# Kernel optimization log

Hardware: AMD Instinct MI355X
Metric: run time of the kernel (lower is better)

## Reference

```python
import jax, jax.numpy as jnp
import numpy as np
from math import sqrt

NUM_CLASSES = 21
TOP_K = 200
CONF_THRESH = 0.01
NMS_THRESH = 0.45
VAR0, VAR1 = 0.1, 0.2
FMAPS = [19, 10, 5, 3, 2, 1]
INPUT_SIZE = 300
STEPS = [16, 32, 64, 100, 150, 300]
MIN_SIZES = [60, 105, 150, 195, 240, 285]
MAX_SIZES = [105, 150, 195, 240, 285, 330]
ASPECT_RATIOS = [[2, 3]] * 6


def _create_priorbox():
    # Faithful numpy port of create_priorbox (runs once at setup).
    mean = []
    for k, f in enumerate(FMAPS):
        f_k = INPUT_SIZE / STEPS[k]
        s_k = MIN_SIZES[k] / INPUT_SIZE
        s_kp = sqrt(s_k * (MAX_SIZES[k] / INPUT_SIZE))
        for i in range(f):
            for j in range(f):
                cx = (j + 0.5) / f_k
                cy = (i + 0.5) / f_k
                mean.append([cx, cy, s_k, s_k])
                mean.append([cx, cy, s_kp, s_kp])
                for ar in ASPECT_RATIOS[k]:
                    r = sqrt(ar)
                    mean.append([cx, cy, s_k * r, s_k / r])
                    mean.append([cx, cy, s_k / r, s_k * r])
    return np.clip(np.asarray(mean, dtype=np.float32), 0.0, 1.0)  # [3000, 4]


def setup_inputs() -> dict:
    key = jax.random.key(0)
    k1, k2 = jax.random.split(key)
    B, P, C = 8, 3000, NUM_CLASSES
    loc_data = jax.random.normal(k1, (B, P, 4), jnp.float32)
    conf_data = jax.random.uniform(k2, (B, P, C), jnp.float32)  # post-softmax-like probs
    priors = jnp.asarray(_create_priorbox())
    return {"loc_data": loc_data, "conf_data": conf_data, "priors": priors}


def _decode(loc, priors):
    # SSD box decode: center-offset form -> corner form. loc, priors: [P, 4]
    cxcy = priors[:, :2] + loc[:, :2] * VAR0 * priors[:, 2:]
    wh = priors[:, 2:] * jnp.exp(loc[:, 2:] * VAR1)
    xy1 = cxcy - 0.5 * wh
    return jnp.concatenate([xy1, xy1 + wh], axis=-1)  # [P, 4] (x1, y1, x2, y2)


def _iou_matrix(b):
    # b: [P, 4] corner-form boxes -> [P, P] pairwise IoU
    area = (b[:, 2] - b[:, 0]) * (b[:, 3] - b[:, 1])
    lt = jnp.maximum(b[:, None, :2], b[None, :, :2])
    rb = jnp.minimum(b[:, None, 2:], b[None, :, 2:])
    wh = jnp.clip(rb - lt, 0.0)
    inter = wh[..., 0] * wh[..., 1]
    union = area[:, None] + area[None, :] - inter
    return inter / jnp.maximum(union, 1e-12)


def _nms_one_class(scores, boxes):
    # scores: [P], boxes: [P, 4]. Greedy hard NMS over threshold-passing boxes,
    # kept detections (in score order) padded to TOP_K rows of [score, x1, y1, x2, y2].
    P = scores.shape[0]
    valid = scores > CONF_THRESH
    s = jnp.where(valid, scores, -jnp.inf)
    order = jnp.argsort(-s)  # descending by score; invalid sorted last
    ss = s[order]
    sb = boxes[order]
    sv = valid[order]
    iou = _iou_matrix(sb)  # [P, P]
    idx = jnp.arange(P)

    def body(i, keep):
        sup = keep[i] & (iou[i] > NMS_THRESH) & (idx > i)
        return keep & ~sup

    keep = jax.lax.stop_gradient(jax.lax.fori_loop(0, P, body, sv))
    # first TOP_K kept candidates, preserving score order
    sel = jnp.argsort(jnp.where(keep, idx, idx + P))[:TOP_K]
    ok = keep[sel]
    out_s = jnp.where(ok, ss[sel], 0.0)
    out_b = jnp.where(ok[:, None], sb[sel], 0.0)
    return jnp.concatenate([out_s[:, None], out_b], axis=-1)  # [TOP_K, 5]


def _per_image(loc, conf, priors):
    boxes = _decode(loc, priors)  # [P, 4]
    cls_scores = conf.T[1:]  # skip background class 0 -> [C-1, P]
    dets = jax.vmap(lambda s: _nms_one_class(s, boxes))(cls_scores)  # [C-1, TOP_K, 5]
    bg = jnp.zeros((1, TOP_K, 5), dets.dtype)
    return jnp.concatenate([bg, dets], axis=0)  # [C, TOP_K, 5]


def reference(loc_data, conf_data, priors):
    # lax.map over batch keeps peak memory to one image's IoU matrices.
    # NOTE: the original's final flt[(rank < top_k)].fill_(0) is a no-op in
    # PyTorch (advanced indexing returns a copy), so output is returned as-is.
    out = jax.lax.map(lambda lc: _per_image(lc[0], lc[1], priors), (loc_data, conf_data))
    return out  # [B, NUM_CLASSES, TOP_K, 5]
```

## Files before the change

### kernel.cpp

```cpp
#include <hip/hip_runtime.h>
#include <math.h>

#pragma clang fp contract(off)

#define PNUM    3000
#define NCLS    21
#define TOPK    200
#define BLOCK   1024
#define CHUNK   1024
#define NMS_T   0.45f
#define LO_BITS 0x3C23D70Bu
#define HI_BITS 0x3F800001u
#define MAXKEEP (TOPK + 64)

__device__ __constant__ unsigned LADDER[15] = {
    0x3F333333u, 0x3F266666u, 0x3F19999Au, 0x3F0CCCCDu, 0x3F000000u,
    0x3EE66666u, 0x3ECCCCCDu, 0x3EB33333u, 0x3E99999Au, 0x3E800000u,
    0x3E4CCCCDu, 0x3E19999Au, 0x3DCCCCCDu, 0x3D4CCCCDu, LO_BITS };

__device__ __forceinline__ float iou_f(float4 a, float aa, float4 b, float ab) {
    float ltx = fmaxf(a.x, b.x);
    float lty = fmaxf(a.y, b.y);
    float rbx = fminf(a.z, b.z);
    float rby = fminf(a.w, b.w);
    float iw  = fmaxf(rbx - ltx, 0.0f);
    float ih  = fmaxf(rby - lty, 0.0f);
    float inter = iw * ih;
    float uni   = aa + ab - inter;
    return inter / fmaxf(uni, 1e-12f);
}

__global__ __launch_bounds__(BLOCK) void ssd_nms_kernel(
    const float* __restrict__ loc,
    const float* __restrict__ conf,
    const float* __restrict__ priors,
    float* __restrict__ out)
{
    const int c   = blockIdx.x;
    const int b   = blockIdx.y;
    const int tid = threadIdx.x;

    float* outbase = out + ((size_t)(b * NCLS + c)) * (TOPK * 5);

    if (c == 0) {
        for (int i = tid; i < TOPK * 5; i += BLOCK) outbase[i] = 0.0f;
        return;
    }

    __shared__ unsigned long long s_bufA[CHUNK];
    __shared__ unsigned long long s_bufB[CHUNK];
    __shared__ float4             s_box[CHUNK];
    __shared__ float              s_area[CHUNK];
    __shared__ float              s_score[CHUNK];
    __shared__ float4             s_kb[MAXKEEP];
    __shared__ float              s_ka[MAXKEEP];
    __shared__ unsigned long long s_supp[64];
    __shared__ int                s_supc[64];
    __shared__ int                s_wcnt[16];
    __shared__ int s_m, s_cnt, s_done;

    const int lane = tid & 63;
    const int wav  = tid >> 6;

    unsigned hb[4];
    const float* confb = conf + ((size_t)b * PNUM) * NCLS + c;
    #pragma unroll
    for (int q = 0; q < 4; ++q) {
        int i = tid + (q << 10);
        unsigned h = 0u;
        if (i < PNUM) {
            float s = confb[(size_t)i * NCLS];
            if (s > 0.01f) h = __float_as_uint(s);
        }
        hb[q] = h;
    }
    if (tid < 64) { s_supp[lane] = 0ull; s_supc[lane] = 0; }
    if (tid == 0) { s_cnt = 0; s_done = 0; }

    unsigned Thi = HI_BITS;
    int rung = 0;
    bool done = false;

    for (;;) {
        unsigned T = LADDER[rung];

        __syncthreads();
        if (tid == 0) s_m = 0;
        s_bufA[tid] = 0ull;
        __syncthreads();
        #pragma unroll
        for (int q = 0; q < 4; ++q) {
            unsigned sb = hb[q];
            bool p = (sb >= T && sb < Thi);
            unsigned long long bal = __ballot(p);
            int wb = 0;
            if (lane == 0 && bal) wb = atomicAdd(&s_m, (int)__popcll(bal));
            wb = __shfl(wb, 0);
            if (p) {
                int dst = wb + (int)__popcll(bal & ((1ull << lane) - 1ull));
                if (dst < CHUNK) {
                    int i = tid + (q << 10);
                    s_bufA[dst] = ((unsigned long long)sb << 32) | (unsigned)(~i);
                }
            }
        }
        __syncthreads();
        int M = s_m;

        if (M > CHUNK) {
            unsigned lo = T + 1, hi = Thi;
            while (lo < hi) {
                unsigned mid = lo + ((hi - lo) >> 1);
                __syncthreads();
                int c2 = 0;
                #pragma unroll
                for (int q = 0; q < 4; ++q)
                    c2 += (int)__popcll(__ballot(hb[q] >= mid && hb[q] < Thi));
                if (lane == 0) s_wcnt[wav] = c2;
                __syncthreads();
                int n = 0;
                #pragma unroll
                for (int w = 0; w < 16; ++w) n += s_wcnt[w];
                if (n <= CHUNK) hi = mid; else lo = mid + 1;
            }
            T = hi;
            __syncthreads();
            int wc = 0;
            #pragma unroll
            for (int q = 0; q < 4; ++q)
                wc += (int)__popcll(__ballot(hb[q] >= T && hb[q] < Thi));
            if (lane == 0) s_wcnt[wav] = wc;
            s_bufA[tid] = 0ull;
            __syncthreads();
            int wbase = 0; M = 0;
            #pragma unroll
            for (int w = 0; w < 16; ++w) {
                int v = s_wcnt[w];
                M += v;
                if (w < wav) wbase += v;
            }
            int base = wbase;
            #pragma unroll
            for (int q = 0; q < 4; ++q) {
                unsigned sb = hb[q];
                bool p = (sb >= T && sb < Thi);
                unsigned long long bal = __ballot(p);
                if (p) {
                    int dst = base + (int)__popcll(bal & ((1ull << lane) - 1ull));
                    int i = tid + (q << 10);
                    s_bufA[dst] = ((unsigned long long)sb << 32) | (unsigned)(~i);
                }
                base += (int)__popcll(bal);
            }
            __syncthreads();
        }

        if (M == 0) {
            if (T <= LO_BITS) break;
            Thi = T;
            while (rung < 14 && LADDER[rung] >= T) rung++;
            continue;
        }

        unsigned N = 64;
        while (N < (unsigned)M) N <<= 1;
        unsigned long long key = s_bufA[tid];
        int parity = 0;
        for (unsigned k = 2; k <= N; k <<= 1) {
            for (unsigned j = k >> 1; j > 0; j >>= 1) {
                unsigned long long pk;
                if (j >= 64) {
                    unsigned long long* buf = parity ? s_bufB : s_bufA;
                    buf[tid] = key;
                    __syncthreads();
                    pk = buf[tid ^ j];
                    parity ^= 1;
                } else {
                    pk = __shfl_xor(key, (int)j, 64);
                }
                bool takeMax  = (((tid & j) == 0) == ((tid & k) == 0));
                bool pGreater = pk > key;
                if (takeMax == pGreater) key = pk;
            }
        }

        if (key != 0ull) {
            unsigned idx = ~(unsigned)key;
            float4 l  = ((const float4*)loc)[(size_t)b * PNUM + idx];
            float4 pr = ((const float4*)priors)[idx];
            float cx = pr.x + l.x * 0.1f * pr.z;
            float cy = pr.y + l.y * 0.1f * pr.w;
            float w  = pr.z * expf(l.z * 0.2f);
            float h  = pr.w * expf(l.w * 0.2f);
            float x1 = cx - 0.5f * w;
            float y1 = cy - 0.5f * h;
            float x2 = x1 + w;
            float y2 = y1 + h;
            s_box[tid]   = make_float4(x1, y1, x2, y2);
            s_area[tid]  = (x2 - x1) * (y2 - y1);
            s_score[tid] = __uint_as_float((unsigned)(key >> 32));
        }
        __syncthreads();

        int pos = 0;
        while (pos < M) {
            int bn  = M - pos; if (bn > 64) bn = 64;
            int cnt = s_cnt;

            if (lane < bn) {
                float4 bL = s_box[pos + lane];
                float  aL = s_area[pos + lane];
                bool bad = false;
                #pragma unroll 2
                for (int K = wav; K < cnt; K += 16)
                    bad |= (iou_f(s_kb[K], s_ka[K], bL, aL) > NMS_T);
                if (bad) s_supc[lane] = 1;
                unsigned long long bits = 0ull;
                int M0 = wav << 2;
                #pragma unroll
                for (int q2 = 0; q2 < 4; ++q2) {
                    int Mi = M0 + q2;
                    if (Mi < lane) {
                        if (iou_f(s_box[pos + Mi], s_area[pos + Mi], bL, aL) > NMS_T)
                            bits |= (1ull << Mi);
                    }
                }
                if (bits) atomicOr(&s_supp[lane], bits);
            }
            __syncthreads();

            if (tid < 64) {
                unsigned long long own      = s_supp[lane];
                unsigned long long deadmask = __ballot(s_supc[lane] != 0);
                bool alive = (lane < bn) && !((deadmask >> lane) & 1ull);
                unsigned long long kept = __ballot(alive && own == 0ull);
                unsigned long long rem0 = __ballot((own & kept) != 0ull);
                unsigned long long cand = __ballot(alive && own != 0ull) & ~rem0;
                while (cand) {
                    int i = __ffsll(cand) - 1;
                    kept |= 1ull << i;
                    unsigned long long vic = __ballot(((own >> i) & 1ull) != 0ull);
                    cand &= ~vic;
                    cand &= ~(1ull << i);
                }
                int keptN = (int)__popcll(kept);
                bool me   = (kept >> lane) & 1ull;
                int krank = (int)__popcll(kept & ((1ull << lane) - 1ull));
                if (me) {
                    int kid = cnt + krank;
                    float4 bx = s_box[pos + lane];
                    s_kb[kid] = bx;
                    s_ka[kid] = s_area[pos + lane];
                    if (kid < TOPK) {
                        float* o = outbase + (size_t)kid * 5;
                        o[0] = s_score[pos + lane];
                        o[1] = bx.x; o[2] = bx.y; o[3] = bx.z; o[4] = bx.w;
                    }
                }
                s_supp[lane] = 0ull;
                s_supc[lane] = 0;
                if (lane == 0) {
                    s_cnt  = cnt + keptN;
                    s_done = (cnt + keptN >= TOPK) ? 1 : 0;
                }
            }
            __syncthreads();
            if (s_done) { done = true; break; }
            pos += bn;
        }

        if (done) break;
        if (T <= LO_BITS) break;
        Thi = T;
        while (rung < 14 && LADDER[rung] >= T) rung++;
    }

    const int cf = s_cnt < TOPK ? s_cnt : TOPK;
    for (int r = cf + tid; r < TOPK; r += BLOCK) {
        float* o = outbase + (size_t)r * 5;
        o[0] = 0.f; o[1] = 0.f; o[2] = 0.f; o[3] = 0.f; o[4] = 0.f;
    }
}

extern "C" void kernel_launch(void* const* d_in, const int* in_sizes, int n_in,
                              void* d_out, int out_size, void* d_ws, size_t ws_size,
                              hipStream_t stream) {
    const float* loc    = (const float*)d_in[0];
    const float* conf   = (const float*)d_in[1];
    const float* priors = (const float*)d_in[2];
    float* out          = (float*)d_out;
    const int B = in_sizes[0] / (PNUM * 4);
    dim3 grid(NCLS, B);
    ssd_nms_kernel<<<grid, BLOCK, 0, stream>>>(loc, conf, priors, out);
}
```

Baseline: 90.03 us.

## Compact surviving candidates after each NMS batch instead of rescanning all kept boxes

After each 64-candidate batch, all remaining candidates in the rung are tested in parallel against only the newly kept boxes. The survivors are then stream-compacted into a ping-pong index buffer, so later batches hold only live candidates and no longer need a per-batch check against every kept box. This removes repeated suppression tests and makes the 64-wide batches denser. In exchange it adds extra block-wide syncs and a prefix-sum pass per batch, and it reuses the sort buffers as index arrays.

```diff
diff --git a/kernel.cpp b/kernel.cpp
--- a/kernel.cpp
+++ b/kernel.cpp
@@ -55,7 +55,6 @@
     __shared__ float4             s_kb[MAXKEEP];
     __shared__ float              s_ka[MAXKEEP];
     __shared__ unsigned long long s_supp[64];
-    __shared__ int                s_supc[64];
     __shared__ int                s_wcnt[16];
     __shared__ int s_m, s_cnt, s_done;
 
@@ -74,7 +73,7 @@
         }
         hb[q] = h;
     }
-    if (tid < 64) { s_supp[lane] = 0ull; s_supc[lane] = 0; }
+    if (tid < 64) s_supp[lane] = 0ull;
     if (tid == 0) { s_cnt = 0; s_done = 0; }
 
     unsigned Thi = HI_BITS;
@@ -200,28 +199,58 @@
             s_area[tid]  = (x2 - x1) * (y2 - y1);
             s_score[tid] = __uint_as_float((unsigned)(key >> 32));
         }
+        unsigned* ibuf = reinterpret_cast<unsigned*>(s_bufA);
+        unsigned* obuf = reinterpret_cast<unsigned*>(s_bufB);
+        if (tid < M) ibuf[tid] = (unsigned)tid;
         __syncthreads();
 
-        int pos = 0;
-        while (pos < M) {
-            int bn  = M - pos; if (bn > 64) bn = 64;
+        int live = M;
+        int nf   = 0;
+        int drop = 0;
+        for (;;) {
             int cnt = s_cnt;
+            if (cnt > nf || drop > 0) {
+                unsigned ci = 0u; bool alive = false;
+                if (tid >= drop && tid < live) {
+                    ci = ibuf[tid];
+                    float4 bL = s_box[ci];
+                    float  aL = s_area[ci];
+                    alive = true;
+                    for (int K = nf; K < cnt; ++K)
+                        alive = alive && !(iou_f(s_kb[K], s_ka[K], bL, aL) > NMS_T);
+                }
+                unsigned long long bal = __ballot(alive);
+                if (lane == 0) s_wcnt[wav] = (int)__popcll(bal);
+                __syncthreads();
+                int base = 0, tot = 0;
+                #pragma unroll
+                for (int w = 0; w < 16; ++w) {
+                    int v = s_wcnt[w];
+                    tot += v;
+                    if (w < wav) base += v;
+                }
+                if (alive)
+                    obuf[base + (int)__popcll(bal & ((1ull << lane) - 1ull))] = ci;
+                unsigned* tsw = ibuf; ibuf = obuf; obuf = tsw;
+                live = tot; nf = cnt; drop = 0;
+                __syncthreads();
+            }
+            if (live == 0) break;
+
+            int bn = live < 64 ? live : 64;
 
             if (lane < bn) {
-                float4 bL = s_box[pos + lane];
-                float  aL = s_area[pos + lane];
-                bool bad = false;
-                #pragma unroll 2
-                for (int K = wav; K < cnt; K += 16)
-                    bad |= (iou_f(s_kb[K], s_ka[K], bL, aL) > NMS_T);
-                if (bad) s_supc[lane] = 1;
+                unsigned ciL = ibuf[lane];
+                float4 bL = s_box[ciL];
+                float  aL = s_area[ciL];
                 unsigned long long bits = 0ull;
                 int M0 = wav << 2;
                 #pragma unroll
                 for (int q2 = 0; q2 < 4; ++q2) {
                     int Mi = M0 + q2;
                     if (Mi < lane) {
-                        if (iou_f(s_box[pos + Mi], s_area[pos + Mi], bL, aL) > NMS_T)
+                        unsigned cj = ibuf[Mi];
+                        if (iou_f(s_box[cj], s_area[cj], bL, aL) > NMS_T)
                             bits |= (1ull << Mi);
                     }
                 }
@@ -230,12 +259,11 @@
             __syncthreads();
 
             if (tid < 64) {
-                unsigned long long own      = s_supp[lane];
-                unsigned long long deadmask = __ballot(s_supc[lane] != 0);
-                bool alive = (lane < bn) && !((deadmask >> lane) & 1ull);
-                unsigned long long kept = __ballot(alive && own == 0ull);
+                unsigned long long own = s_supp[lane];
+                bool aliv = (lane < bn);
+                unsigned long long kept = __ballot(aliv && own == 0ull);
                 unsigned long long rem0 = __ballot((own & kept) != 0ull);
-                unsigned long long cand = __ballot(alive && own != 0ull) & ~rem0;
+                unsigned long long cand = __ballot(aliv && own != 0ull) & ~rem0;
                 while (cand) {
                     int i = __ffsll(cand) - 1;
                     kept |= 1ull << i;
@@ -246,27 +274,28 @@
                 int keptN = (int)__popcll(kept);
                 bool me   = (kept >> lane) & 1ull;
                 int krank = (int)__popcll(kept & ((1ull << lane) - 1ull));
+                int cnt0  = s_cnt;
                 if (me) {
-                    int kid = cnt + krank;
-                    float4 bx = s_box[pos + lane];
+                    int kid = cnt0 + krank;
+                    unsigned ciL = ibuf[lane];
+                    float4 bx = s_box[ciL];
                     s_kb[kid] = bx;
-                    s_ka[kid] = s_area[pos + lane];
+                    s_ka[kid] = s_area[ciL];
                     if (kid < TOPK) {
                         float* o = outbase + (size_t)kid * 5;
-                        o[0] = s_score[pos + lane];
+                        o[0] = s_score[ciL];
                         o[1] = bx.x; o[2] = bx.y; o[3] = bx.z; o[4] = bx.w;
                     }
                 }
                 s_supp[lane] = 0ull;
-                s_supc[lane] = 0;
                 if (lane == 0) {
-                    s_cnt  = cnt + keptN;
-                    s_done = (cnt + keptN >= TOPK) ? 1 : 0;
+                    s_cnt  = cnt0 + keptN;
+                    s_done = (cnt0 + keptN >= TOPK) ? 1 : 0;
                 }
             }
             __syncthreads();
             if (s_done) { done = true; break; }
-            pos += bn;
+            drop = bn;
         }
 
         if (done) break;
```

Measured after the change: 115.8 us. +28.6%, slower.
